# Kernel optimization log

Measured on AMD Instinct MI355X. Metric: run time of the kernel, lower is better.

Reference implementation:

```python
import jax, jax.numpy as jnp
import numpy as np

MODEL_DIM = 512
COND_DIM = 768
HEAD_DIM = 64
N_HEADS = 8


def setup_inputs() -> dict:
    key = jax.random.key(0)
    k1, k2, k3, k4, k5, k6 = jax.random.split(key, 6)
    inner = HEAD_DIM * N_HEADS
    x = jax.random.normal(k1, (16, 4096, MODEL_DIM), dtype=jnp.float32)
    cond = jax.random.normal(k2, (16, 77, COND_DIM), dtype=jnp.float32)
    # nn.Linear weights (out, in); apply as x @ W.T
    s = 0.02
    w_q = jax.random.normal(k3, (inner, MODEL_DIM), dtype=jnp.float32) * s
    w_k = jax.random.normal(k4, (inner, COND_DIM), dtype=jnp.float32) * s
    w_v = jax.random.normal(k5, (inner, COND_DIM), dtype=jnp.float32) * s
    w_o = jax.random.normal(k6, (MODEL_DIM, inner), dtype=jnp.float32) * s
    return {"x": x, "cond": cond, "w_q": w_q, "w_k": w_k, "w_v": w_v, "w_o": w_o}


def reference(x, cond, w_q, w_k, w_v, w_o):
    b, lq, _ = x.shape
    lk = cond.shape[1]
    q = (x @ w_q.T).reshape(b, lq, N_HEADS, HEAD_DIM)
    k = (cond @ w_k.T).reshape(b, lk, N_HEADS, HEAD_DIM)
    v = (cond @ w_v.T).reshape(b, lk, N_HEADS, HEAD_DIM)
    scale = HEAD_DIM ** -0.5
    attn = jnp.einsum('bihd,bjhd->bhij', q, k) * scale  # [b,h,lq,lk]
    attn = jax.nn.softmax(attn, axis=-1)
    out = jnp.einsum('bhij,bjhd->bihd', attn, v).reshape(b, lq, N_HEADS * HEAD_DIM)
    return out @ w_o.T
```

## Files before the change

### kernel.cpp

```cpp
#include <hip/hip_runtime.h>
#include <hip/hip_bf16.h>
#include <stdint.h>


typedef __bf16 bf16_t;
typedef __bf16 bf16x8 __attribute__((ext_vector_type(8)));
typedef float floatx4 __attribute__((ext_vector_type(4)));

#define MFMA16(a, b, c) __builtin_amdgcn_mfma_f32_16x16x32_bf16((a), (b), (c), 0, 0, 0)

__device__ __forceinline__ void gload_lds16(const bf16_t* g, bf16_t* l)
{
    __builtin_amdgcn_global_load_lds(
        (const __attribute__((address_space(1))) void*)g,
        (__attribute__((address_space(3))) void*)l, 16, 0, 0);
}

__global__ __launch_bounds__(256) void cvt_big(
    const float* __restrict__ in, bf16_t* __restrict__ out, long long n8)
{
    for (long long i = (long long)blockIdx.x * 256 + threadIdx.x; i < n8;
         i += (long long)gridDim.x * 256) {
        floatx4 f0 = *(const floatx4*)(in + i * 8);
        floatx4 f1 = *(const floatx4*)(in + i * 8 + 4);
        bf16x8 v;
#pragma unroll
        for (int e = 0; e < 4; e++) { v[e] = (bf16_t)f0[e]; v[e + 4] = (bf16_t)f1[e]; }
        *(bf16x8*)(out + i * 8) = v;
    }
}

struct Cvt5 {
    const float* s[5];
    bf16_t* d[5];
    int n8[5];
};

__global__ __launch_bounds__(256) void cvt_multi(Cvt5 c)
{
    const int seg = blockIdx.y;
    const long long i = (long long)blockIdx.x * 256 + threadIdx.x;
    if (i >= c.n8[seg]) return;
    const float* in = c.s[seg];
    bf16_t* out = c.d[seg];
    floatx4 f0 = *(const floatx4*)(in + i * 8);
    floatx4 f1 = *(const floatx4*)(in + i * 8 + 4);
    bf16x8 v;
#pragma unroll
    for (int e = 0; e < 4; e++) { v[e] = (bf16_t)f0[e]; v[e + 4] = (bf16_t)f1[e]; }
    *(bf16x8*)(out + i * 8) = v;
}

template <bool CF32>
__global__ __launch_bounds__(256) void gemm_bt(
    const bf16_t* __restrict__ A, const bf16_t* __restrict__ B,
    void* __restrict__ Cv, int M, int N, int K)
{
    __shared__ bf16_t As[128 * 32];
    __shared__ bf16_t Bs[128 * 32];

    const int t = threadIdx.x;
    const int l = t & 63;
    const int w = t >> 6;
    const int wm = w >> 1, wn = w & 1;
    const int l15 = l & 15, l4 = l >> 4;
    const int m0 = blockIdx.y * 128, n0 = blockIdx.x * 128;

    floatx4 acc[4][4] = {};

    const bf16_t* ag[2];
    const bf16_t* bg[2];
    bf16_t* al[2];
    bf16_t* bl[2];
#pragma unroll
    for (int i = 0; i < 2; i++) {
        int e = (i * 256 + t) * 8;
        int row = e >> 5, col = e & 31;
        int ra = m0 + row; if (ra > M - 1) ra = M - 1;
        ag[i] = A + (size_t)ra * K + col;
        bg[i] = B + (size_t)(n0 + row) * K + col;
        al[i] = &As[e];
        bl[i] = &Bs[e];
    }

    for (int k0 = 0; k0 < K; k0 += 32) {
#pragma unroll
        for (int i = 0; i < 2; i++) {
            gload_lds16(ag[i] + k0, al[i]);
            gload_lds16(bg[i] + k0, bl[i]);
        }
        __syncthreads();

        bf16x8 af[4], bfr[4];
#pragma unroll
        for (int i = 0; i < 4; i++)
            af[i] = *(const bf16x8*)&As[(wm * 64 + i * 16 + l15) * 32 + l4 * 8];
#pragma unroll
        for (int j = 0; j < 4; j++)
            bfr[j] = *(const bf16x8*)&Bs[(wn * 64 + j * 16 + l15) * 32 + l4 * 8];
#pragma unroll
        for (int i = 0; i < 4; i++)
#pragma unroll
            for (int j = 0; j < 4; j++)
                acc[i][j] = MFMA16(af[i], bfr[j], acc[i][j]);
        __syncthreads();
    }

#pragma unroll
    for (int i = 0; i < 4; i++)
#pragma unroll
        for (int j = 0; j < 4; j++)
#pragma unroll
            for (int r = 0; r < 4; r++) {
                int row = m0 + wm * 64 + i * 16 + l4 * 4 + r;
                int col = n0 + wn * 64 + j * 16 + l15;
                if (row < M) {
                    if (CF32) ((float*)Cv)[(size_t)row * N + col] = acc[i][j][r];
                    else ((bf16_t*)Cv)[(size_t)row * N + col] = (bf16_t)acc[i][j][r];
                }
            }
}

#define LK 77
#define KSTR 72
#define VSTR 104
#define JP 96

__global__ __launch_bounds__(256) void attn_fused(
    bf16_t* QO,
    const bf16_t* __restrict__ Kg,
    const bf16_t* __restrict__ Vg)
{
    __shared__ bf16_t Ks[80 * KSTR];
    __shared__ bf16_t Vs[64 * VSTR];
    __shared__ bf16_t Ps[4 * 16 * VSTR];

    const int t = threadIdx.x;
    const int w = t >> 6, l = t & 63;
    const int l15 = l & 15, l4 = l >> 4;
    const int b = blockIdx.y >> 3, h = blockIdx.y & 7;
    const int q0 = blockIdx.x * 64;

    for (int idx = t; idx < LK * 8; idx += 256) {
        int j = idx >> 3, c = (idx & 7) * 8;
        *(uint4*)&Ks[j * KSTR + c] =
            *(const uint4*)&Kg[((size_t)(b * LK + j)) * 512 + h * 64 + c];
    }
    for (int idx = t; idx < 3 * KSTR; idx += 256)
        Ks[LK * KSTR + idx] = (bf16_t)0.0f;

    for (int idx = t; idx < LK * 64; idx += 256) {
        int j = idx >> 6, d = idx & 63;
        Vs[d * VSTR + j] = Vg[((size_t)(b * LK + j)) * 512 + h * 64 + d];
    }
    for (int idx = t; idx < 64 * (JP - LK); idx += 256) {
        int d = idx / (JP - LK), j = LK + idx % (JP - LK);
        Vs[d * VSTR + j] = (bf16_t)0.0f;
    }
    __syncthreads();

    const bf16_t* qbase =
        QO + ((size_t)(b * 4096 + q0 + w * 16 + l15)) * 512 + h * 64 + l4 * 8;
    bf16x8 aq0 = *(const bf16x8*)qbase;
    bf16x8 aq1 = *(const bf16x8*)(qbase + 32);

    floatx4 s[5];
#pragma unroll
    for (int n = 0; n < 5; n++) {
        floatx4 z = {0.f, 0.f, 0.f, 0.f};
        bf16x8 b0 = *(const bf16x8*)&Ks[(n * 16 + l15) * KSTR + l4 * 8];
        bf16x8 b1 = *(const bf16x8*)&Ks[(n * 16 + l15) * KSTR + 32 + l4 * 8];
        z = MFMA16(aq0, b0, z);
        z = MFMA16(aq1, b1, z);
        s[n] = z;
    }

    const float scale = 0.125f;
    float p[5][4], linv[4];
#pragma unroll
    for (int r = 0; r < 4; r++) {
        float smax = -1e30f;
#pragma unroll
        for (int n = 0; n < 5; n++) {
            float v = s[n][r] * scale;
            if (n == 4 && (64 + l15) >= LK) v = -1e30f;
            p[n][r] = v;
            smax = fmaxf(smax, v);
        }
#pragma unroll
        for (int off = 1; off < 16; off <<= 1)
            smax = fmaxf(smax, __shfl_xor(smax, off, 64));
        float sum = 0.f;
#pragma unroll
        for (int n = 0; n < 5; n++) {
            float e = __expf(p[n][r] - smax);
            p[n][r] = e;
            sum += e;
        }
#pragma unroll
        for (int off = 1; off < 16; off <<= 1)
            sum += __shfl_xor(sum, off, 64);
        linv[r] = 1.0f / sum;
    }

    bf16_t* pw = Ps + w * 16 * VSTR;
#pragma unroll
    for (int r = 0; r < 4; r++) {
        int row = l4 * 4 + r;
#pragma unroll
        for (int n = 0; n < 5; n++)
            pw[row * VSTR + n * 16 + l15] = (bf16_t)(p[n][r] * linv[r]);
        pw[row * VSTR + 80 + l15] = (bf16_t)0.0f;
    }
    __syncthreads();

    bf16x8 ap[3];
#pragma unroll
    for (int ks = 0; ks < 3; ks++)
        ap[ks] = *(const bf16x8*)&pw[l15 * VSTR + ks * 32 + l4 * 8];
#pragma unroll
    for (int n2 = 0; n2 < 4; n2++) {
        floatx4 o = {0.f, 0.f, 0.f, 0.f};
#pragma unroll
        for (int ks = 0; ks < 3; ks++) {
            bf16x8 bv = *(const bf16x8*)&Vs[(n2 * 16 + l15) * VSTR + ks * 32 + l4 * 8];
            o = MFMA16(ap[ks], bv, o);
        }
#pragma unroll
        for (int r = 0; r < 4; r++) {
            int q = q0 + w * 16 + l4 * 4 + r;
            QO[((size_t)(b * 4096 + q)) * 512 + h * 64 + n2 * 16 + l15] = (bf16_t)o[r];
        }
    }
}

extern "C" void kernel_launch(void* const* d_in, const int* in_sizes, int n_in,
                              void* d_out, int out_size, void* d_ws, size_t ws_size,
                              hipStream_t stream)
{
    const float* x    = (const float*)d_in[0];
    const float* cond = (const float*)d_in[1];
    const float* w_q  = (const float*)d_in[2];
    const float* w_k  = (const float*)d_in[3];
    const float* w_v  = (const float*)d_in[4];
    const float* w_o  = (const float*)d_in[5];
    float* out = (float*)d_out;

    const int Mq  = 16 * 4096;
    const int Mkv = 16 * 77;

    bf16_t* Qb  = (bf16_t*)d_ws;
    bf16_t* Kb  = Qb + (size_t)Mq * 512;
    bf16_t* Vb  = Kb + (size_t)Mkv * 512;
    bf16_t* Wob = Vb + (size_t)Mkv * 512;

    bf16_t* Xb  = (bf16_t*)d_out;
    bf16_t* Cb  = Xb  + (size_t)Mq * 512;
    bf16_t* Wqb = Cb  + (size_t)Mkv * 768;
    bf16_t* Wkb = Wqb + (size_t)512 * 512;
    bf16_t* Wvb = Wkb + (size_t)512 * 768;

    const long long n8x = (long long)Mq * 512 / 8;
    cvt_big<<<dim3(2048), 256, 0, stream>>>(x, Xb, n8x);

    Cvt5 c;
    c.s[0] = cond; c.d[0] = Cb;  c.n8[0] = Mkv * 768 / 8;
    c.s[1] = w_q;  c.d[1] = Wqb; c.n8[1] = 512 * 512 / 8;
    c.s[2] = w_k;  c.d[2] = Wkb; c.n8[2] = 512 * 768 / 8;
    c.s[3] = w_v;  c.d[3] = Wvb; c.n8[3] = 512 * 768 / 8;
    c.s[4] = w_o;  c.d[4] = Wob; c.n8[4] = 512 * 512 / 8;
    cvt_multi<<<dim3((118272 + 255) / 256, 5), 256, 0, stream>>>(c);

    gemm_bt<false><<<dim3(4, Mq / 128), 256, 0, stream>>>(Xb, Wqb, Qb, Mq, 512, 512);
    gemm_bt<false><<<dim3(4, (Mkv + 127) / 128), 256, 0, stream>>>(Cb, Wkb, Kb, Mkv, 512, 768);
    gemm_bt<false><<<dim3(4, (Mkv + 127) / 128), 256, 0, stream>>>(Cb, Wvb, Vb, Mkv, 512, 768);

    attn_fused<<<dim3(64, 128), 256, 0, stream>>>(Qb, Kb, Vb);

    gemm_bt<true><<<dim3(4, Mq / 128), 256, 0, stream>>>(Qb, Wob, out, Mq, 512, 512);
}
```

Before: 449.8 us.

## Process 128 queries per attention block to amortize K/V staging

Each attention block now handles 128 query rows (32 per wave, two 16-row MFMA tiles) instead of 64, so the per-(batch,head) K/V load and transpose into LDS is done half as often. The V transpose load is vectorized with 16-byte global reads, Q loads are issued before the LDS staging to overlap latency, and s_setprio is raised around MFMA bursts. This costs more registers and LDS per block and halves the grid size, which may reduce occupancy.

```diff
diff --git a/kernel.cpp b/kernel.cpp
--- a/kernel.cpp
+++ b/kernel.cpp
@@ -133,13 +133,21 @@
 {
     __shared__ bf16_t Ks[80 * KSTR];
     __shared__ bf16_t Vs[64 * VSTR];
-    __shared__ bf16_t Ps[4 * 16 * VSTR];
+    __shared__ bf16_t Ps[4 * 32 * VSTR];
 
     const int t = threadIdx.x;
     const int w = t >> 6, l = t & 63;
     const int l15 = l & 15, l4 = l >> 4;
     const int b = blockIdx.y >> 3, h = blockIdx.y & 7;
-    const int q0 = blockIdx.x * 64;
+    const int q0 = blockIdx.x * 128;
+
+    const bf16_t* qbase =
+        QO + ((size_t)(b * 4096 + q0 + w * 32 + l15)) * 512 + h * 64 + l4 * 8;
+    bf16x8 aq[2][2];
+    aq[0][0] = *(const bf16x8*)qbase;
+    aq[0][1] = *(const bf16x8*)(qbase + 32);
+    aq[1][0] = *(const bf16x8*)(qbase + 16 * 512);
+    aq[1][1] = *(const bf16x8*)(qbase + 16 * 512 + 32);
 
     for (int idx = t; idx < LK * 8; idx += 256) {
         int j = idx >> 3, c = (idx & 7) * 8;
@@ -149,9 +157,13 @@
     for (int idx = t; idx < 3 * KSTR; idx += 256)
         Ks[LK * KSTR + idx] = (bf16_t)0.0f;
 
-    for (int idx = t; idx < LK * 64; idx += 256) {
-        int j = idx >> 6, d = idx & 63;
-        Vs[d * VSTR + j] = Vg[((size_t)(b * LK + j)) * 512 + h * 64 + d];
+    for (int u = t; u < LK * 8; u += 256) {
+        int j = u >> 3, d0 = (u & 7) * 8;
+        uint4 pk = *(const uint4*)&Vg[((size_t)(b * LK + j)) * 512 + h * 64 + d0];
+        const bf16_t* pv = (const bf16_t*)&pk;
+#pragma unroll
+        for (int e = 0; e < 8; e++)
+            Vs[(d0 + e) * VSTR + j] = pv[e];
     }
     for (int idx = t; idx < 64 * (JP - LK); idx += 256) {
         int d = idx / (JP - LK), j = LK + idx % (JP - LK);
@@ -159,78 +171,96 @@
     }
     __syncthreads();
 
-    const bf16_t* qbase =
-        QO + ((size_t)(b * 4096 + q0 + w * 16 + l15)) * 512 + h * 64 + l4 * 8;
-    bf16x8 aq0 = *(const bf16x8*)qbase;
-    bf16x8 aq1 = *(const bf16x8*)(qbase + 32);
-
-    floatx4 s[5];
+    floatx4 s[2][5];
+    __builtin_amdgcn_s_setprio(1);
 #pragma unroll
     for (int n = 0; n < 5; n++) {
-        floatx4 z = {0.f, 0.f, 0.f, 0.f};
         bf16x8 b0 = *(const bf16x8*)&Ks[(n * 16 + l15) * KSTR + l4 * 8];
         bf16x8 b1 = *(const bf16x8*)&Ks[(n * 16 + l15) * KSTR + 32 + l4 * 8];
-        z = MFMA16(aq0, b0, z);
-        z = MFMA16(aq1, b1, z);
-        s[n] = z;
-    }
+#pragma unroll
+        for (int mi = 0; mi < 2; mi++) {
+            floatx4 z = {0.f, 0.f, 0.f, 0.f};
+            z = MFMA16(aq[mi][0], b0, z);
+            z = MFMA16(aq[mi][1], b1, z);
+            s[mi][n] = z;
+        }
+    }
+    __builtin_amdgcn_s_setprio(0);
 
     const float scale = 0.125f;
-    float p[5][4], linv[4];
-#pragma unroll
-    for (int r = 0; r < 4; r++) {
-        float smax = -1e30f;
-#pragma unroll
-        for (int n = 0; n < 5; n++) {
-            float v = s[n][r] * scale;
-            if (n == 4 && (64 + l15) >= LK) v = -1e30f;
-            p[n][r] = v;
-            smax = fmaxf(smax, v);
-        }
-#pragma unroll
-        for (int off = 1; off < 16; off <<= 1)
-            smax = fmaxf(smax, __shfl_xor(smax, off, 64));
-        float sum = 0.f;
-#pragma unroll
-        for (int n = 0; n < 5; n++) {
-            float e = __expf(p[n][r] - smax);
-            p[n][r] = e;
-            sum += e;
-        }
-#pragma unroll
-        for (int off = 1; off < 16; off <<= 1)
-            sum += __shfl_xor(sum, off, 64);
-        linv[r] = 1.0f / sum;
-    }
-
-    bf16_t* pw = Ps + w * 16 * VSTR;
-#pragma unroll
-    for (int r = 0; r < 4; r++) {
-        int row = l4 * 4 + r;
-#pragma unroll
-        for (int n = 0; n < 5; n++)
-            pw[row * VSTR + n * 16 + l15] = (bf16_t)(p[n][r] * linv[r]);
-        pw[row * VSTR + 80 + l15] = (bf16_t)0.0f;
-    }
+    float p[2][5][4], linv[2][4];
+#pragma unroll
+    for (int mi = 0; mi < 2; mi++)
+#pragma unroll
+        for (int r = 0; r < 4; r++) {
+            float smax = -1e30f;
+#pragma unroll
+            for (int n = 0; n < 5; n++) {
+                float v = s[mi][n][r] * scale;
+                if (n == 4 && (64 + l15) >= LK) v = -1e30f;
+                p[mi][n][r] = v;
+                smax = fmaxf(smax, v);
+            }
+#pragma unroll
+            for (int off = 1; off < 16; off <<= 1)
+                smax = fmaxf(smax, __shfl_xor(smax, off, 64));
+            float sum = 0.f;
+#pragma unroll
+            for (int n = 0; n < 5; n++) {
+                float e2 = __expf(p[mi][n][r] - smax);
+                p[mi][n][r] = e2;
+                sum += e2;
+            }
+#pragma unroll
+            for (int off = 1; off < 16; off <<= 1)
+                sum += __shfl_xor(sum, off, 64);
+            linv[mi][r] = 1.0f / sum;
+        }
+
+    bf16_t* pw = Ps + w * 32 * VSTR;
+#pragma unroll
+    for (int mi = 0; mi < 2; mi++)
+#pragma unroll
+        for (int r = 0; r < 4; r++) {
+            int row = mi * 16 + l4 * 4 + r;
+#pragma unroll
+            for (int n = 0; n < 5; n++)
+                pw[row * VSTR + n * 16 + l15] = (bf16_t)(p[mi][n][r] * linv[mi][r]);
+            pw[row * VSTR + 80 + l15] = (bf16_t)0.0f;
+        }
     __syncthreads();
 
-    bf16x8 ap[3];
-#pragma unroll
-    for (int ks = 0; ks < 3; ks++)
-        ap[ks] = *(const bf16x8*)&pw[l15 * VSTR + ks * 32 + l4 * 8];
+    bf16x8 ap[2][3];
+#pragma unroll
+    for (int mi = 0; mi < 2; mi++)
+#pragma unroll
+        for (int ks = 0; ks < 3; ks++)
+            ap[mi][ks] = *(const bf16x8*)&pw[(mi * 16 + l15) * VSTR + ks * 32 + l4 * 8];
 #pragma unroll
     for (int n2 = 0; n2 < 4; n2++) {
-        floatx4 o = {0.f, 0.f, 0.f, 0.f};
-#pragma unroll
-        for (int ks = 0; ks < 3; ks++) {
-            bf16x8 bv = *(const bf16x8*)&Vs[(n2 * 16 + l15) * VSTR + ks * 32 + l4 * 8];
-            o = MFMA16(ap[ks], bv, o);
-        }
-#pragma unroll
-        for (int r = 0; r < 4; r++) {
-            int q = q0 + w * 16 + l4 * 4 + r;
-            QO[((size_t)(b * 4096 + q)) * 512 + h * 64 + n2 * 16 + l15] = (bf16_t)o[r];
-        }
+        bf16x8 bv[3];
+#pragma unroll
+        for (int ks = 0; ks < 3; ks++)
+            bv[ks] = *(const bf16x8*)&Vs[(n2 * 16 + l15) * VSTR + ks * 32 + l4 * 8];
+        floatx4 o[2];
+        __builtin_amdgcn_s_setprio(1);
+#pragma unroll
+        for (int mi = 0; mi < 2; mi++) {
+            floatx4 z = {0.f, 0.f, 0.f, 0.f};
+#pragma unroll
+            for (int ks = 0; ks < 3; ks++)
+                z = MFMA16(ap[mi][ks], bv[ks], z);
+            o[mi] = z;
+        }
+        __builtin_amdgcn_s_setprio(0);
+#pragma unroll
+        for (int mi = 0; mi < 2; mi++)
+#pragma unroll
+            for (int r = 0; r < 4; r++) {
+                int q = q0 + w * 32 + mi * 16 + l4 * 4 + r;
+                QO[((size_t)(b * 4096 + q)) * 512 + h * 64 + n2 * 16 + l15] =
+                    (bf16_t)o[mi][r];
+            }
     }
 }
 
@@ -275,7 +305,7 @@
     gemm_bt<false><<<dim3(4, (Mkv + 127) / 128), 256, 0, stream>>>(Cb, Wkb, Kb, Mkv, 512, 768);
     gemm_bt<false><<<dim3(4, (Mkv + 127) / 128), 256, 0, stream>>>(Cb, Wvb, Vb, Mkv, 512, 768);
 
-    attn_fused<<<dim3(64, 128), 256, 0, stream>>>(Qb, Kb, Vb);
+    attn_fused<<<dim3(32, 128), 256, 0, stream>>>(Qb, Kb, Vb);
 
     gemm_bt<true><<<dim3(4, Mq / 128), 256, 0, stream>>>(Qb, Wob, out, Mq, 512, 512);
 }
```

Measured after the change: 445.2 us. Within noise of the previous version (-1.0%).
